# Performance work log

Measured on AMD Instinct MI355X. Metric: run time of the kernel, lower is better.

The kernel has to match this reference:

```python
import jax, jax.numpy as jnp
import numpy as np

N_SRC0, N_DST0 = 400000, 100000
N_DST1 = 25000


def _graph_conv(x_src, src, dst, n_dst, W, b):
    # DGL GraphConv, norm='both': h_v = d_in(v)^-1/2 * sum_{u->v} d_out(u)^-1/2 * x_u @ W + b
    ones = jnp.ones(src.shape[0], dtype=x_src.dtype)
    out_deg = jax.ops.segment_sum(ones, src, num_segments=x_src.shape[0])
    in_deg = jax.ops.segment_sum(ones, dst, num_segments=n_dst)
    cs = jnp.where(out_deg > 0, out_deg ** -0.5, 0.0).astype(x_src.dtype)
    cd = jnp.where(in_deg > 0, in_deg ** -0.5, 0.0).astype(x_src.dtype)
    msg = (x_src * cs[:, None])[src]                      # [E, d_in] gather
    agg = jax.ops.segment_sum(msg, dst, num_segments=n_dst)  # [n_dst, d_in] scatter-add
    return (agg * cd[:, None]) @ W + b


def setup_inputs() -> dict:
    key = jax.random.key(0)
    ks = jax.random.split(key, 8)
    E0, E1 = 3200000, 800000
    return {
        "x": jax.random.normal(ks[0], (N_SRC0, 128), dtype=jnp.float32),
        "src0": jax.random.randint(ks[1], (E0,), 0, N_SRC0, dtype=jnp.int32),
        "dst0": jax.random.randint(ks[2], (E0,), 0, N_DST0, dtype=jnp.int32),
        "src1": jax.random.randint(ks[3], (E1,), 0, N_DST0, dtype=jnp.int32),
        "dst1": jax.random.randint(ks[4], (E1,), 0, N_DST1, dtype=jnp.int32),
        "W0": jax.random.normal(ks[5], (128, 256), dtype=jnp.float32) * (128 ** -0.5),
        "b0": jnp.zeros((256,), dtype=jnp.float32),
        "W1": jax.random.normal(ks[6], (256, 64), dtype=jnp.float32) * (256 ** -0.5),
        "b1": jnp.zeros((64,), dtype=jnp.float32),
    }


def reference(x, src0, dst0, src1, dst1, W0, b0, W1, b1):
    h = jax.nn.relu(_graph_conv(x, src0, dst0, N_DST0, W0, b0))   # [N_DST0, 256]
    h = jax.nn.relu(_graph_conv(h, src1, dst1, N_DST1, W1, b1))   # [N_DST1, 64]
    return h
```

## Files before the change

kernel.cpp:

```cpp
#include <hip/hip_runtime.h>
#include <hip/hip_bf16.h>
#include <hip/hip_fp16.h>
#include <stdint.h>

#define N_SRC0 400000
#define N_DST0 100000
#define N_DST1 25000

#define SH_D0 9
#define NK_D0 196
#define SH_S0 9
#define NK_S0 782
#define SH_D1 8
#define NK_D1 98
#define SH_S1 9
#define NK_S1 196
#define NB0 512
#define NB1 128

#define BH_D0 0
#define BH_S0 (NK_D0 * NB0)
#define BH_D1 (BH_S0 + NK_S0 * NB0)
#define BH_S1 (BH_D1 + NK_D1 * NB1)
#define BH_TOT (BH_S1 + NK_S1 * NB1)

typedef __attribute__((ext_vector_type(8))) short short8;
typedef __attribute__((ext_vector_type(4))) float f32x4;

__device__ __forceinline__ unsigned short f2bf(float f) {
    __hip_bfloat16 h = __float2bfloat16(f);
    union { __hip_bfloat16 h; unsigned short u; } c;
    c.h = h;
    return c.u;
}
__device__ __forceinline__ uint32_t packbf2(float a, float b) {
    return (uint32_t)f2bf(a) | ((uint32_t)f2bf(b) << 16);
}
__device__ __forceinline__ __half2 u2h2(uint32_t u) {
    return __builtin_bit_cast(__half2, u);
}

__device__ __forceinline__ void hist_body(
        const int* __restrict__ src, const int* __restrict__ dst, int n,
        int sshift, int snb, int dshift, int dnb, int NB, int blk,
        int* __restrict__ bhd, int* __restrict__ bhs, int* h) {
    for (int i = threadIdx.x; i < dnb + snb; i += 256) h[i] = 0;
    __syncthreads();
    const int per = (n + NB - 1) / NB;
    const int b = blk * per;
    const int e = min(b + per, n);
    for (int i = b + threadIdx.x; i < e; i += 256) {
        atomicAdd(&h[dst[i] >> dshift], 1);
        atomicAdd(&h[dnb + (src[i] >> sshift)], 1);
    }
    __syncthreads();
    for (int i = threadIdx.x; i < dnb; i += 256) bhd[(size_t)i * NB + blk] = h[i];
    for (int i = threadIdx.x; i < snb; i += 256) bhs[(size_t)i * NB + blk] = h[dnb + i];
}

__global__ __launch_bounds__(256) void hist_fused(
        const int* __restrict__ src0, const int* __restrict__ dst0, int E0,
        const int* __restrict__ src1, const int* __restrict__ dst1, int E1,
        int* __restrict__ bh) {
    extern __shared__ int h[];
    if (blockIdx.x < NB0)
        hist_body(src0, dst0, E0, SH_S0, NK_S0, SH_D0, NK_D0, NB0, blockIdx.x,
                  bh + BH_D0, bh + BH_S0, h);
    else
        hist_body(src1, dst1, E1, SH_S1, NK_S1, SH_D1, NK_D1, NB1, blockIdx.x - NB0,
                  bh + BH_D1, bh + BH_S1, h);
}

#define SCAN_ITEMS 8
#define SCAN_TILE 2048

__global__ __launch_bounds__(256) void scan1_kernel(
        const int* __restrict__ in, int* __restrict__ out,
        int* __restrict__ sums, int n) {
    __shared__ int lds[256];
    const int tid = threadIdx.x;
    const int base = blockIdx.x * SCAN_TILE + tid * SCAN_ITEMS;
    int v[SCAN_ITEMS];
    int run = 0;
    #pragma unroll
    for (int i = 0; i < SCAN_ITEMS; ++i) {
        int t = (base + i < n) ? in[base + i] : 0;
        v[i] = run;
        run += t;
    }
    lds[tid] = run;
    __syncthreads();
    int incl = run;
    for (int off = 1; off < 256; off <<= 1) {
        int u = (tid >= off) ? lds[tid - off] : 0;
        __syncthreads();
        incl += u;
        lds[tid] = incl;
        __syncthreads();
    }
    if (tid == 255) sums[blockIdx.x] = incl;
    int excl = incl - run;
    #pragma unroll
    for (int i = 0; i < SCAN_ITEMS; ++i)
        if (base + i < n) out[base + i] = excl + v[i];
}

__global__ __launch_bounds__(256) void scan2_kernel(int* __restrict__ sums, int nb) {
    __shared__ int lds[256];
    const int tid = threadIdx.x;
    const int base = tid * 4;
    int v[4];
    int run = 0;
    #pragma unroll
    for (int i = 0; i < 4; ++i) {
        int t = (base + i < nb) ? sums[base + i] : 0;
        v[i] = run;
        run += t;
    }
    lds[tid] = run;
    __syncthreads();
    int incl = run;
    for (int off = 1; off < 256; off <<= 1) {
        int u = (tid >= off) ? lds[tid - off] : 0;
        __syncthreads();
        incl += u;
        lds[tid] = incl;
        __syncthreads();
    }
    int excl = incl - run;
    #pragma unroll
    for (int i = 0; i < 4; ++i)
        if (base + i < nb) sums[base + i] = excl + v[i];
}

__device__ __forceinline__ void scat_body(
        const int* __restrict__ src, const int* __restrict__ dst, int n,
        int sshift, int snb, int dshift, int dnb, int NB, int blk, int ksh,
        const int* __restrict__ bhd, const int* __restrict__ bhs,
        const int* __restrict__ sums, int goffd, int goffs, int Td, int Ts,
        uint32_t* __restrict__ stg_d, unsigned short* __restrict__ stg_s, int* cur) {
    for (int i = threadIdx.x; i < dnb; i += 256) {
        int gi = goffd + i * NB + blk;
        cur[i] = bhd[(size_t)i * NB + blk] + sums[gi >> 11] - Td;
    }
    for (int i = threadIdx.x; i < snb; i += 256) {
        int gi = goffs + i * NB + blk;
        cur[dnb + i] = bhs[(size_t)i * NB + blk] + sums[gi >> 11] - Ts;
    }
    __syncthreads();
    const int per = (n + NB - 1) / NB;
    const int b = blk * per;
    const int e = min(b + per, n);
    const int dmask = (1 << dshift) - 1;
    const int smask = (1 << sshift) - 1;
    for (int i = b + threadIdx.x; i < e; i += 256) {
        int s = src[i], d = dst[i];
        int pd = atomicAdd(&cur[d >> dshift], 1);
        stg_d[pd] = ((uint32_t)(d & dmask) << ksh) | (uint32_t)s;
        int ps = atomicAdd(&cur[dnb + (s >> sshift)], 1);
        stg_s[ps] = (unsigned short)(s & smask);
    }
}

__global__ __launch_bounds__(256) void scat_fused(
        const int* __restrict__ src0, const int* __restrict__ dst0, int E0,
        const int* __restrict__ src1, const int* __restrict__ dst1, int E1,
        const int* __restrict__ bh, const int* __restrict__ sums,
        uint32_t* __restrict__ stgd0, unsigned short* __restrict__ stgs0,
        uint32_t* __restrict__ stgd1, unsigned short* __restrict__ stgs1) {
    extern __shared__ int cur[];
    if (blockIdx.x < NB0)
        scat_body(src0, dst0, E0, SH_S0, NK_S0, SH_D0, NK_D0, NB0, blockIdx.x, 19,
                  bh + BH_D0, bh + BH_S0, sums, BH_D0, BH_S0, 0, E0,
                  stgd0, stgs0, cur);
    else
        scat_body(src1, dst1, E1, SH_S1, NK_S1, SH_D1, NK_D1, NB1, blockIdx.x - NB0, 17,
                  bh + BH_D1, bh + BH_S1, sums, BH_D1, BH_S1, 2 * E0, 2 * E0 + E1,
                  stgd1, stgs1, cur);
}

__device__ __forceinline__ int fold_base(const int* bht, const int* sums,
                                         int goff, int NB, int T, int k) {
    int gi = goff + k * NB;
    return bht[(size_t)k * NB] + sums[gi >> 11] - T;
}

__device__ __forceinline__ void fine_csr_body(
        const uint32_t* __restrict__ stg, const int* __restrict__ bht,
        const int* __restrict__ sums, int goff, int T,
        int NB, int shift, int ksh, int nbins, int total, int nbkt, int k,
        int* __restrict__ off, int* __restrict__ esrc, int* fine, int* part) {
    const int fb = 1 << shift;
    const int base = fold_base(bht, sums, goff, NB, T, k);
    const int end = (k + 1 < nbkt) ? fold_base(bht, sums, goff, NB, T, k + 1) : total;
    const int gb = k << shift;
    const int t = threadIdx.x;
    const uint32_t mask = (1u << ksh) - 1;
    for (int i = t; i < fb; i += 256) fine[i] = 0;
    __syncthreads();
    for (int i = base + t; i < end; i += 256)
        atomicAdd(&fine[stg[i] >> ksh], 1);
    __syncthreads();
    int a0 = (2 * t < fb) ? fine[2 * t] : 0;
    int a1 = (2 * t + 1 < fb) ? fine[2 * t + 1] : 0;
    part[t] = a0 + a1;
    __syncthreads();
    int incl = part[t];
    for (int o = 1; o < 256; o <<= 1) {
        int u = (t >= o) ? part[t - o] : 0;
        __syncthreads();
        incl += u;
        part[t] = incl;
        __syncthreads();
    }
    int excl = incl - (a0 + a1);
    if (2 * t < fb) fine[2 * t] = excl;
    if (2 * t + 1 < fb) fine[2 * t + 1] = excl + a0;
    __syncthreads();
    for (int i = t; i < fb; i += 256) {
        int g = gb + i;
        if (g < nbins) off[g] = base + fine[i];
    }
    if (k == nbkt - 1 && t == 0) off[nbins] = total;
    __syncthreads();
    for (int i = base + t; i < end; i += 256) {
        uint32_t v = stg[i];
        int p = atomicAdd(&fine[v >> ksh], 1);
        esrc[base + p] = (int)(v & mask);
    }
}

__device__ __forceinline__ void fine_deg_body(
        const unsigned short* __restrict__ stg, const int* __restrict__ bht,
        const int* __restrict__ sums, int goff, int T,
        int NB, int shift, int nbins, int total, int nbkt, int k,
        float* __restrict__ csf, int* fine) {
    const int fb = 1 << shift;
    const int base = fold_base(bht, sums, goff, NB, T, k);
    const int end = (k + 1 < nbkt) ? fold_base(bht, sums, goff, NB, T, k + 1) : total;
    const int gb = k << shift;
    for (int i = threadIdx.x; i < fb; i += 256) fine[i] = 0;
    __syncthreads();
    for (int i = base + threadIdx.x; i < end; i += 256)
        atomicAdd(&fine[stg[i]], 1);
    __syncthreads();
    for (int i = threadIdx.x; i < fb; i += 256) {
        int g = gb + i;
        if (g < nbins) {
            int c = fine[i];
            csf[g] = c > 0 ? rsqrtf((float)c) : 0.f;
        }
    }
}

__global__ __launch_bounds__(256) void fine_fused(
        const uint32_t* __restrict__ stgd0, const unsigned short* __restrict__ stgs0,
        const uint32_t* __restrict__ stgd1, const unsigned short* __restrict__ stgs1,
        const int* __restrict__ bh, const int* __restrict__ sums,
        int E0, int E1,
        int* __restrict__ off0, int* __restrict__ esrc0,
        int* __restrict__ off1, int* __restrict__ esrc1,
        float* __restrict__ cs0, float* __restrict__ cs1,
        const float* __restrict__ W0, const float* __restrict__ W1,
        unsigned short* __restrict__ W0p, unsigned short* __restrict__ W1p) {
    __shared__ int fine[512];
    __shared__ int part[256];
    int kb = blockIdx.x;
    if (kb < NK_D0) {
        fine_csr_body(stgd0, bh + BH_D0, sums, BH_D0, 0,
                      NB0, SH_D0, 19, N_DST0, E0, NK_D0, kb, off0, esrc0, fine, part);
        return;
    }
    kb -= NK_D0;
    if (kb < NK_S0) {
        fine_deg_body(stgs0, bh + BH_S0, sums, BH_S0, E0,
                      NB0, SH_S0, N_SRC0, E0, NK_S0, kb, cs0, fine);
        return;
    }
    kb -= NK_S0;
    if (kb < NK_D1) {
        fine_csr_body(stgd1, bh + BH_D1, sums, BH_D1, 2 * E0,
                      NB1, SH_D1, 17, N_DST1, E1, NK_D1, kb, off1, esrc1, fine, part);
        return;
    }
    kb -= NK_D1;
    if (kb < NK_S1) {
        fine_deg_body(stgs1, bh + BH_S1, sums, BH_S1, 2 * E0 + E1,
                      NB1, SH_S1, N_DST0, E1, NK_S1, kb, cs1, fine);
        return;
    }
    kb -= NK_S1;
    if (kb < 128) {
        int id = kb * 256 + threadIdx.x;
        int kk = id & 31, n2 = (id >> 5) & 255, kt = id >> 13;
        W0p[id] = f2bf(W0[(kt * 32 + kk) * 256 + n2]);
    } else {
        int id = (kb - 128) * 256 + threadIdx.x;
        int kk = id & 31, n2 = (id >> 5) & 63, kt = id >> 11;
        W1p[id] = f2bf(W1[(kt * 32 + kk) * 64 + n2]);
    }
}

__global__ __launch_bounds__(256) void prescale_kernel(
        const float4* __restrict__ x4, const float* __restrict__ cs,
        uint2* __restrict__ xs) {
    int id = blockIdx.x * 256 + threadIdx.x;
    int row = id >> 5;
    float c = cs[row];
    float4 v = x4[id];
    uint2 o;
    o.x = __builtin_bit_cast(uint32_t, __floats2half2_rn(v.x * c, v.y * c));
    o.y = __builtin_bit_cast(uint32_t, __floats2half2_rn(v.z * c, v.w * c));
    xs[id] = o;
}

__global__ __launch_bounds__(256) void agg0_kernel(
        const uint32_t* __restrict__ xs, const int* __restrict__ esrc,
        const int* __restrict__ off, uint32_t* __restrict__ aggb) {
    const int row = blockIdx.x * 4 + (threadIdx.x >> 6);
    const uint32_t t = threadIdx.x & 63;
    const int b = off[row], e = off[row + 1];
    const __half2 z = __builtin_bit_cast(__half2, 0u);
    __half2 a[16];
    #pragma unroll
    for (int k = 0; k < 16; ++k) a[k] = z;
    int i = b;
    for (; i + 15 < e; i += 16) {
        uint32_t idx[16];
        #pragma unroll
        for (int k = 0; k < 16; ++k)
            idx[k] = ((uint32_t)esrc[i + k] << 6) + t;
        #pragma unroll
        for (int k = 0; k < 16; ++k)
            a[k] = __hadd2(a[k], u2h2(xs[idx[k]]));
    }
    for (; i + 3 < e; i += 4) {
        #pragma unroll
        for (int k = 0; k < 4; ++k)
            a[k] = __hadd2(a[k], u2h2(xs[((uint32_t)esrc[i + k] << 6) + t]));
    }
    for (; i < e; ++i)
        a[0] = __hadd2(a[0], u2h2(xs[((uint32_t)esrc[i] << 6) + t]));
    #pragma unroll
    for (int k = 0; k < 8; ++k) a[k] = __hadd2(a[k], a[k + 8]);
    #pragma unroll
    for (int k = 0; k < 4; ++k) a[k] = __hadd2(a[k], a[k + 4]);
    __half2 s = __hadd2(__hadd2(a[0], a[1]), __hadd2(a[2], a[3]));
    float cd = (e > b) ? rsqrtf((float)(e - b)) : 0.f;
    aggb[(size_t)row * 64 + t] = packbf2(__low2float(s) * cd, __high2float(s) * cd);
}

__global__ __launch_bounds__(256) void gemm01_mfma(
        const short* __restrict__ A,
        const short* __restrict__ B0p,
        const float* __restrict__ bias0,
        const short* __restrict__ B1p,
        const float* __restrict__ cs1,
        __half* __restrict__ Y) {
    __shared__ short hs[32][264];
    const int w = threadIdx.x >> 6;
    const int l = threadIdx.x & 63;
    const int rbase = blockIdx.x * 32;
    const int lr = l & 15;
    const int lk = (l >> 4) * 8;
    const int orow0 = (l >> 4) * 4;

    {
        const int cbase = w * 64;
        f32x4 acc[2][4] = {};
        #pragma unroll
        for (int kt = 0; kt < 4; ++kt) {
            short8 a[2], b[4];
            #pragma unroll
            for (int rt = 0; rt < 2; ++rt)
                a[rt] = *(const short8*)(A + (size_t)(rbase + rt * 16 + lr) * 128 + kt * 32 + lk);
            #pragma unroll
            for (int ct = 0; ct < 4; ++ct)
                b[ct] = *(const short8*)(B0p + (size_t)(kt * 256 + cbase + ct * 16 + lr) * 32 + lk);
            #pragma unroll
            for (int rt = 0; rt < 2; ++rt)
                #pragma unroll
                for (int ct = 0; ct < 4; ++ct)
                    acc[rt][ct] = __builtin_amdgcn_mfma_f32_16x16x32_bf16(a[rt], b[ct], acc[rt][ct], 0, 0, 0);
        }
        #pragma unroll
        for (int rt = 0; rt < 2; ++rt) {
            #pragma unroll
            for (int ct = 0; ct < 4; ++ct) {
                int col = cbase + ct * 16 + lr;
                float bv = bias0[col];
                #pragma unroll
                for (int j = 0; j < 4; ++j)
                    hs[rt * 16 + orow0 + j][col] = (short)f2bf(fmaxf(acc[rt][ct][j] + bv, 0.f));
            }
        }
    }
    __syncthreads();

    {
        f32x4 acc2[2] = {};
        #pragma unroll
        for (int kt = 0; kt < 8; ++kt) {
            short8 b1 = *(const short8*)(B1p + (size_t)(kt * 64 + w * 16 + lr) * 32 + lk);
            #pragma unroll
            for (int rt = 0; rt < 2; ++rt) {
                short8 av = *(const short8*)(&hs[rt * 16 + lr][kt * 32 + lk]);
                acc2[rt] = __builtin_amdgcn_mfma_f32_16x16x32_bf16(av, b1, acc2[rt], 0, 0, 0);
            }
        }
        #pragma unroll
        for (int rt = 0; rt < 2; ++rt) {
            #pragma unroll
            for (int j = 0; j < 4; ++j) {
                int row = rbase + rt * 16 + orow0 + j;
                float c = cs1[row];
                Y[(size_t)row * 64 + w * 16 + lr] = __float2half(acc2[rt][j] * c);
            }
        }
    }
}

__global__ __launch_bounds__(256) void agg1_kernel(
        const uint2* __restrict__ y2, const int* __restrict__ esrc,
        const int* __restrict__ off, const float* __restrict__ bias,
        float* __restrict__ out, int nrows) {
    int row = blockIdx.x * 16 + (threadIdx.x >> 4);
    int t = threadIdx.x & 15;
    if (row >= nrows) return;
    int b = off[row], e = off[row + 1];
    const __half2 z = __builtin_bit_cast(__half2, 0u);
    __half2 aA0 = z, aA1 = z, aB0 = z, aB1 = z;
    int i = b;
    for (; i + 8 <= e; i += 8) {
        #pragma unroll
        for (int k = 0; k < 8; k += 2) {
            int s0 = esrc[i + k], s1 = esrc[i + k + 1];
            uint2 v0 = y2[(size_t)s0 * 16 + t];
            uint2 v1 = y2[(size_t)s1 * 16 + t];
            aA0 = __hadd2(aA0, u2h2(v0.x));
            aA1 = __hadd2(aA1, u2h2(v0.y));
            aB0 = __hadd2(aB0, u2h2(v1.x));
            aB1 = __hadd2(aB1, u2h2(v1.y));
        }
    }
    for (; i < e; ++i) {
        uint2 v = y2[(size_t)esrc[i] * 16 + t];
        aA0 = __hadd2(aA0, u2h2(v.x));
        aA1 = __hadd2(aA1, u2h2(v.y));
    }
    float cd = (e > b) ? rsqrtf((float)(e - b)) : 0.f;
    __half2 s0 = __hadd2(aA0, aB0), s1 = __hadd2(aA1, aB1);
    float4 bv = *(const float4*)(bias + t * 4);
    float4 o;
    o.x = fmaxf(__low2float(s0) * cd + bv.x, 0.f);
    o.y = fmaxf(__high2float(s0) * cd + bv.y, 0.f);
    o.z = fmaxf(__low2float(s1) * cd + bv.z, 0.f);
    o.w = fmaxf(__high2float(s1) * cd + bv.w, 0.f);
    *(float4*)(out + (size_t)row * 64 + t * 4) = o;
}

extern "C" void kernel_launch(void* const* d_in, const int* in_sizes, int n_in,
                              void* d_out, int out_size, void* d_ws, size_t ws_size,
                              hipStream_t stream) {
    const float* x    = (const float*)d_in[0];
    const int*   src0 = (const int*)d_in[1];
    const int*   dst0 = (const int*)d_in[2];
    const int*   src1 = (const int*)d_in[3];
    const int*   dst1 = (const int*)d_in[4];
    const float* W0   = (const float*)d_in[5];
    const float* b0   = (const float*)d_in[6];
    const float* W1   = (const float*)d_in[7];
    const float* b1   = (const float*)d_in[8];
    float* out = (float*)d_out;

    const int E0 = in_sizes[1];
    const int E1 = in_sizes[3];

    char* p = (char*)d_ws;
    auto alloc = [&](size_t bytes) {
        char* r = p;
        p += (bytes + 511) & ~(size_t)511;
        return r;
    };
    int*   bh    = (int*)alloc((size_t)BH_TOT * 4);
    int*   sums  = (int*)alloc(1024 * 4);
    int*   off0  = (int*)alloc((size_t)(N_DST0 + 1) * 4);
    int*   off1  = (int*)alloc((size_t)(N_DST1 + 1) * 4);
    float* cs0   = (float*)alloc((size_t)N_SRC0 * 4);
    float* cs1   = (float*)alloc((size_t)N_DST0 * 4);
    int*   esrc0 = (int*)alloc((size_t)E0 * 4);
    int*   esrc1 = (int*)alloc((size_t)E1 * 4);
    unsigned short* W0p = (unsigned short*)alloc((size_t)32768 * 2);
    unsigned short* W1p = (unsigned short*)alloc((size_t)16384 * 2);
    size_t bigA = (size_t)N_SRC0 * 128 * 2;
    size_t bigB = (size_t)N_DST0 * 128 * 2;
    size_t bigStg = (size_t)(E0 * 6 + E1 * 6 + 1024);
    size_t bigSz = bigA + bigB;
    if (bigStg > bigSz) bigSz = bigStg;
    char* big = alloc(bigSz);

    char* q = big;
    auto carve = [&](size_t bytes) {
        char* r = q;
        q += (bytes + 511) & ~(size_t)511;
        return r;
    };
    uint32_t*       stgd0 = (uint32_t*)carve((size_t)E0 * 4);
    unsigned short* stgs0 = (unsigned short*)carve((size_t)E0 * 2);
    uint32_t*       stgd1 = (uint32_t*)carve((size_t)E1 * 4);
    unsigned short* stgs1 = (unsigned short*)carve((size_t)E1 * 2);

    uint2*    xs   = (uint2*)big;
    __half*   y1b  = (__half*)big;
    uint32_t* aggb = (uint32_t*)(big + bigA);

    hist_fused<<<NB0 + NB1, 256, (NK_D0 + NK_S0) * 4, stream>>>(
        src0, dst0, E0, src1, dst1, E1, bh);
    const int nsb = (BH_TOT + SCAN_TILE - 1) / SCAN_TILE;
    scan1_kernel<<<nsb, 256, 0, stream>>>(bh, bh, sums, BH_TOT);
    scan2_kernel<<<1, 256, 0, stream>>>(sums, nsb);
    scat_fused<<<NB0 + NB1, 256, (NK_D0 + NK_S0) * 4, stream>>>(
        src0, dst0, E0, src1, dst1, E1, bh, sums, stgd0, stgs0, stgd1, stgs1);
    fine_fused<<<NK_D0 + NK_S0 + NK_D1 + NK_S1 + 192, 256, 0, stream>>>(
        stgd0, stgs0, stgd1, stgs1, bh, sums, E0, E1,
        off0, esrc0, off1, esrc1, cs0, cs1, W0, W1, W0p, W1p);

    prescale_kernel<<<N_SRC0 * 32 / 256, 256, 0, stream>>>((const float4*)x, cs0, xs);

    agg0_kernel<<<N_DST0 / 4, 256, 0, stream>>>(
        (const uint32_t*)xs, esrc0, off0, aggb);

    gemm01_mfma<<<N_DST0 / 32, 256, 0, stream>>>(
        (const short*)aggb, (const short*)W0p, b0, (const short*)W1p, cs1, y1b);

    agg1_kernel<<<(N_DST1 + 15) / 16, 256, 0, stream>>>(
        (const uint2*)y1b, esrc1, off1, b1, out, N_DST1);
}
```

Before: 381.4 us.

## Shrink fine buckets to 256 bins, store source keys as bytes, unroll fine loops

The coarse bucket width for the graph-0 destination and both source degree passes drops from 512 to 256 bins, which doubles the bucket counts. The source staging keys can then be stored as uint8 instead of uint16, halving that staging traffic. The fine histogram and CSR-fill kernels now assume one bin per thread, drop the pair-wise scan, and unroll the edge loops four-wide for more memory-level parallelism. In exchange, the histogram and scan arrays grow, the scatter needs more LDS per block, and the fine pass launches more blocks with less work each.

```diff
diff --git a/kernel.cpp b/kernel.cpp
--- a/kernel.cpp
+++ b/kernel.cpp
@@ -7,14 +7,14 @@
 #define N_DST0 100000
 #define N_DST1 25000
 
-#define SH_D0 9
-#define NK_D0 196
-#define SH_S0 9
-#define NK_S0 782
+#define SH_D0 8
+#define NK_D0 391
+#define SH_S0 8
+#define NK_S0 1563
 #define SH_D1 8
 #define NK_D1 98
-#define SH_S1 9
-#define NK_S1 196
+#define SH_S1 8
+#define NK_S1 391
 #define NB0 512
 #define NB1 128
 
@@ -138,7 +138,7 @@
         int sshift, int snb, int dshift, int dnb, int NB, int blk, int ksh,
         const int* __restrict__ bhd, const int* __restrict__ bhs,
         const int* __restrict__ sums, int goffd, int goffs, int Td, int Ts,
-        uint32_t* __restrict__ stg_d, unsigned short* __restrict__ stg_s, int* cur) {
+        uint32_t* __restrict__ stg_d, uint8_t* __restrict__ stg_s, int* cur) {
     for (int i = threadIdx.x; i < dnb; i += 256) {
         int gi = goffd + i * NB + blk;
         cur[i] = bhd[(size_t)i * NB + blk] + sums[gi >> 11] - Td;
@@ -152,13 +152,12 @@
     const int b = blk * per;
     const int e = min(b + per, n);
     const int dmask = (1 << dshift) - 1;
-    const int smask = (1 << sshift) - 1;
     for (int i = b + threadIdx.x; i < e; i += 256) {
         int s = src[i], d = dst[i];
         int pd = atomicAdd(&cur[d >> dshift], 1);
         stg_d[pd] = ((uint32_t)(d & dmask) << ksh) | (uint32_t)s;
         int ps = atomicAdd(&cur[dnb + (s >> sshift)], 1);
-        stg_s[ps] = (unsigned short)(s & smask);
+        stg_s[ps] = (uint8_t)(s & 255);
     }
 }
 
@@ -166,8 +165,8 @@
         const int* __restrict__ src0, const int* __restrict__ dst0, int E0,
         const int* __restrict__ src1, const int* __restrict__ dst1, int E1,
         const int* __restrict__ bh, const int* __restrict__ sums,
-        uint32_t* __restrict__ stgd0, unsigned short* __restrict__ stgs0,
-        uint32_t* __restrict__ stgd1, unsigned short* __restrict__ stgs1) {
+        uint32_t* __restrict__ stgd0, uint8_t* __restrict__ stgs0,
+        uint32_t* __restrict__ stgd1, uint8_t* __restrict__ stgs1) {
     extern __shared__ int cur[];
     if (blockIdx.x < NB0)
         scat_body(src0, dst0, E0, SH_S0, NK_S0, SH_D0, NK_D0, NB0, blockIdx.x, 19,
@@ -188,24 +187,31 @@
 __device__ __forceinline__ void fine_csr_body(
         const uint32_t* __restrict__ stg, const int* __restrict__ bht,
         const int* __restrict__ sums, int goff, int T,
-        int NB, int shift, int ksh, int nbins, int total, int nbkt, int k,
+        int NB, int ksh, int nbins, int total, int nbkt, int k,
         int* __restrict__ off, int* __restrict__ esrc, int* fine, int* part) {
-    const int fb = 1 << shift;
+    const int fb = 256;
     const int base = fold_base(bht, sums, goff, NB, T, k);
     const int end = (k + 1 < nbkt) ? fold_base(bht, sums, goff, NB, T, k + 1) : total;
-    const int gb = k << shift;
+    const int gb = k << 8;
     const int t = threadIdx.x;
     const uint32_t mask = (1u << ksh) - 1;
-    for (int i = t; i < fb; i += 256) fine[i] = 0;
-    __syncthreads();
-    for (int i = base + t; i < end; i += 256)
+    fine[t] = 0;
+    __syncthreads();
+    int i = base + t;
+    for (; i + 768 < end; i += 1024) {
+        uint32_t v0 = stg[i], v1 = stg[i + 256], v2 = stg[i + 512], v3 = stg[i + 768];
+        atomicAdd(&fine[v0 >> ksh], 1);
+        atomicAdd(&fine[v1 >> ksh], 1);
+        atomicAdd(&fine[v2 >> ksh], 1);
+        atomicAdd(&fine[v3 >> ksh], 1);
+    }
+    for (; i < end; i += 256)
         atomicAdd(&fine[stg[i] >> ksh], 1);
     __syncthreads();
-    int a0 = (2 * t < fb) ? fine[2 * t] : 0;
-    int a1 = (2 * t + 1 < fb) ? fine[2 * t + 1] : 0;
-    part[t] = a0 + a1;
-    __syncthreads();
-    int incl = part[t];
+    int a = fine[t];
+    part[t] = a;
+    __syncthreads();
+    int incl = a;
     for (int o = 1; o < 256; o <<= 1) {
         int u = (t >= o) ? part[t - o] : 0;
         __syncthreads();
@@ -213,17 +219,27 @@
         part[t] = incl;
         __syncthreads();
     }
-    int excl = incl - (a0 + a1);
-    if (2 * t < fb) fine[2 * t] = excl;
-    if (2 * t + 1 < fb) fine[2 * t + 1] = excl + a0;
-    __syncthreads();
-    for (int i = t; i < fb; i += 256) {
-        int g = gb + i;
-        if (g < nbins) off[g] = base + fine[i];
-    }
-    if (k == nbkt - 1 && t == 0) off[nbins] = total;
-    __syncthreads();
-    for (int i = base + t; i < end; i += 256) {
+    fine[t] = incl - a;
+    __syncthreads();
+    {
+        int g = gb + t;
+        if (g < nbins) off[g] = base + fine[t];
+        if (k == nbkt - 1 && t == 0) off[nbins] = total;
+    }
+    __syncthreads();
+    i = base + t;
+    for (; i + 768 < end; i += 1024) {
+        uint32_t v0 = stg[i], v1 = stg[i + 256], v2 = stg[i + 512], v3 = stg[i + 768];
+        int p0 = atomicAdd(&fine[v0 >> ksh], 1);
+        esrc[base + p0] = (int)(v0 & mask);
+        int p1 = atomicAdd(&fine[v1 >> ksh], 1);
+        esrc[base + p1] = (int)(v1 & mask);
+        int p2 = atomicAdd(&fine[v2 >> ksh], 1);
+        esrc[base + p2] = (int)(v2 & mask);
+        int p3 = atomicAdd(&fine[v3 >> ksh], 1);
+        esrc[base + p3] = (int)(v3 & mask);
+    }
+    for (; i < end; i += 256) {
         uint32_t v = stg[i];
         int p = atomicAdd(&fine[v >> ksh], 1);
         esrc[base + p] = (int)(v & mask);
@@ -231,31 +247,37 @@
 }
 
 __device__ __forceinline__ void fine_deg_body(
-        const unsigned short* __restrict__ stg, const int* __restrict__ bht,
+        const uint8_t* __restrict__ stg, const int* __restrict__ bht,
         const int* __restrict__ sums, int goff, int T,
-        int NB, int shift, int nbins, int total, int nbkt, int k,
+        int NB, int nbins, int total, int nbkt, int k,
         float* __restrict__ csf, int* fine) {
-    const int fb = 1 << shift;
     const int base = fold_base(bht, sums, goff, NB, T, k);
     const int end = (k + 1 < nbkt) ? fold_base(bht, sums, goff, NB, T, k + 1) : total;
-    const int gb = k << shift;
-    for (int i = threadIdx.x; i < fb; i += 256) fine[i] = 0;
-    __syncthreads();
-    for (int i = base + threadIdx.x; i < end; i += 256)
+    const int gb = k << 8;
+    const int t = threadIdx.x;
+    fine[t] = 0;
+    __syncthreads();
+    int i = base + t;
+    for (; i + 768 < end; i += 1024) {
+        uint32_t v0 = stg[i], v1 = stg[i + 256], v2 = stg[i + 512], v3 = stg[i + 768];
+        atomicAdd(&fine[v0], 1);
+        atomicAdd(&fine[v1], 1);
+        atomicAdd(&fine[v2], 1);
+        atomicAdd(&fine[v3], 1);
+    }
+    for (; i < end; i += 256)
         atomicAdd(&fine[stg[i]], 1);
     __syncthreads();
-    for (int i = threadIdx.x; i < fb; i += 256) {
-        int g = gb + i;
-        if (g < nbins) {
-            int c = fine[i];
-            csf[g] = c > 0 ? rsqrtf((float)c) : 0.f;
-        }
+    int g = gb + t;
+    if (g < nbins) {
+        int c = fine[t];
+        csf[g] = c > 0 ? rsqrtf((float)c) : 0.f;
     }
 }
 
 __global__ __launch_bounds__(256) void fine_fused(
-        const uint32_t* __restrict__ stgd0, const unsigned short* __restrict__ stgs0,
-        const uint32_t* __restrict__ stgd1, const unsigned short* __restrict__ stgs1,
+        const uint32_t* __restrict__ stgd0, const uint8_t* __restrict__ stgs0,
+        const uint32_t* __restrict__ stgd1, const uint8_t* __restrict__ stgs1,
         const int* __restrict__ bh, const int* __restrict__ sums,
         int E0, int E1,
         int* __restrict__ off0, int* __restrict__ esrc0,
@@ -263,30 +285,30 @@
         float* __restrict__ cs0, float* __restrict__ cs1,
         const float* __restrict__ W0, const float* __restrict__ W1,
         unsigned short* __restrict__ W0p, unsigned short* __restrict__ W1p) {
-    __shared__ int fine[512];
+    __shared__ int fine[256];
     __shared__ int part[256];
     int kb = blockIdx.x;
     if (kb < NK_D0) {
         fine_csr_body(stgd0, bh + BH_D0, sums, BH_D0, 0,
-                      NB0, SH_D0, 19, N_DST0, E0, NK_D0, kb, off0, esrc0, fine, part);
+                      NB0, 19, N_DST0, E0, NK_D0, kb, off0, esrc0, fine, part);
         return;
     }
     kb -= NK_D0;
     if (kb < NK_S0) {
         fine_deg_body(stgs0, bh + BH_S0, sums, BH_S0, E0,
-                      NB0, SH_S0, N_SRC0, E0, NK_S0, kb, cs0, fine);
+                      NB0, N_SRC0, E0, NK_S0, kb, cs0, fine);
         return;
     }
     kb -= NK_S0;
     if (kb < NK_D1) {
         fine_csr_body(stgd1, bh + BH_D1, sums, BH_D1, 2 * E0,
-                      NB1, SH_D1, 17, N_DST1, E1, NK_D1, kb, off1, esrc1, fine, part);
+                      NB1, 17, N_DST1, E1, NK_D1, kb, off1, esrc1, fine, part);
         return;
     }
     kb -= NK_D1;
     if (kb < NK_S1) {
         fine_deg_body(stgs1, bh + BH_S1, sums, BH_S1, 2 * E0 + E1,
-                      NB1, SH_S1, N_DST0, E1, NK_S1, kb, cs1, fine);
+                      NB1, N_DST0, E1, NK_S1, kb, cs1, fine);
         return;
     }
     kb -= NK_S1;
@@ -494,10 +516,7 @@
     unsigned short* W1p = (unsigned short*)alloc((size_t)16384 * 2);
     size_t bigA = (size_t)N_SRC0 * 128 * 2;
     size_t bigB = (size_t)N_DST0 * 128 * 2;
-    size_t bigStg = (size_t)(E0 * 6 + E1 * 6 + 1024);
-    size_t bigSz = bigA + bigB;
-    if (bigStg > bigSz) bigSz = bigStg;
-    char* big = alloc(bigSz);
+    char* big = alloc(bigA + bigB);
 
     char* q = big;
     auto carve = [&](size_t bytes) {
@@ -505,10 +524,10 @@
         q += (bytes + 511) & ~(size_t)511;
         return r;
     };
-    uint32_t*       stgd0 = (uint32_t*)carve((size_t)E0 * 4);
-    unsigned short* stgs0 = (unsigned short*)carve((size_t)E0 * 2);
-    uint32_t*       stgd1 = (uint32_t*)carve((size_t)E1 * 4);
-    unsigned short* stgs1 = (unsigned short*)carve((size_t)E1 * 2);
+    uint32_t* stgd0 = (uint32_t*)carve((size_t)E0 * 4);
+    uint8_t*  stgs0 = (uint8_t*)carve((size_t)E0);
+    uint32_t* stgd1 = (uint32_t*)carve((size_t)E1 * 4);
+    uint8_t*  stgs1 = (uint8_t*)carve((size_t)E1);
 
     uint2*    xs   = (uint2*)big;
     __half*   y1b  = (__half*)big;
```

Measured after the change: 384.7 us. Within noise of the previous version (+0.9%).
